# Optimization experiments

Hardware: AMD Instinct MI355X
Metric: run time of the kernel (lower is better)

Reference implementation:

```python
import jax, jax.numpy as jnp
import numpy as np
import math

H = 16          # n_head
N_EMBD = 1024
EPS = 1e-5      # torch LayerNorm default


def setup_inputs() -> dict:
    key = jax.random.key(0)
    ks = jax.random.split(key, 6)
    B, T, C = 2, 2048, 1024
    x = jax.random.normal(ks[0], (B, T, C), dtype=jnp.float32)
    s = 0.02  # GPT-2 style init scale keeps softmax logits sane
    Wq = jax.random.normal(ks[1], (C, N_EMBD), dtype=jnp.float32) * s
    Wk = jax.random.normal(ks[2], (C, N_EMBD), dtype=jnp.float32) * s
    Wv = jax.random.normal(ks[3], (C, N_EMBD), dtype=jnp.float32) * s
    Wo = jax.random.normal(ks[4], (N_EMBD, C), dtype=jnp.float32) * s
    return {
        "x": x,
        "Wq": Wq, "bq": jnp.zeros((N_EMBD,), jnp.float32),
        "Wk": Wk, "bk": jnp.zeros((N_EMBD,), jnp.float32),
        "Wv": Wv, "bv": jnp.zeros((N_EMBD,), jnp.float32),
        "Wo": Wo, "bo": jnp.zeros((C,), jnp.float32),
        "gamma": jnp.ones((C,), jnp.float32),
        "beta": jnp.zeros((C,), jnp.float32),
    }


def reference(x, Wq, bq, Wk, bk, Wv, bv, Wo, bo, gamma, beta):
    B, T, _ = x.shape
    Dh = N_EMBD // H
    # projections -> (B, H, T, Dh)
    def split_heads(y):
        return y.reshape(B, T, H, Dh).transpose(0, 2, 1, 3)
    q = split_heads(x @ Wq + bq)
    k = split_heads(x @ Wk + bk)
    v = split_heads(x @ Wv + bv)
    # naive causal attention: explicit (B,H,T,T) scores
    att = jnp.einsum("bhtd,bhsd->bhts", q, k) * (1.0 / math.sqrt(Dh))
    causal = jnp.tril(jnp.ones((T, T), dtype=bool))
    att = jnp.where(causal[None, None], att, -jnp.inf)
    att = jax.nn.softmax(att, axis=-1)
    o = jnp.einsum("bhts,bhsd->bhtd", att, v)
    o = o.transpose(0, 2, 1, 3).reshape(B, T, N_EMBD)
    y = o @ Wo + bo
    # LayerNorm (dropout is identity at p=0 / eval)
    mu = jnp.mean(y, axis=-1, keepdims=True)
    var = jnp.var(y, axis=-1, keepdims=True)
    return (y - mu) * jax.lax.rsqrt(var + EPS) * gamma + beta
```

## Files before the change

kernel.cpp:

```cpp
#include <hip/hip_runtime.h>
#include <stdint.h>
#include <stddef.h>

typedef __attribute__((ext_vector_type(8))) short short8;
typedef __attribute__((ext_vector_type(4))) float f32x4;
typedef __attribute__((ext_vector_type(16))) float f32x16;
typedef __attribute__((ext_vector_type(4))) unsigned short us4;
typedef __attribute__((ext_vector_type(4))) unsigned u32x4;

#define DEVI static __device__ __forceinline__

DEVI unsigned short f2bf(float f) {
  unsigned u = __builtin_bit_cast(unsigned, f);
  u += 0x7FFFu + ((u >> 16) & 1u);
  return (unsigned short)(u >> 16);
}

DEVI float bf2f(unsigned short u) {
  return __builtin_bit_cast(float, ((unsigned)u) << 16);
}

DEVI f32x4 mfma16(short8 a, short8 b, f32x4 c) {
  return __builtin_amdgcn_mfma_f32_16x16x32_bf16(a, b, c, 0, 0, 0);
}

DEVI f32x16 mfma32(short8 a, short8 b, f32x16 c) {
  return __builtin_amdgcn_mfma_f32_32x32x16_bf16(a, b, c, 0, 0, 0);
}

DEVI unsigned cvtpk(float lo, float hi) {
  unsigned r;
  asm("v_cvt_pk_bf16_f32 %0, %1, %2" : "=v"(r) : "v"(lo), "v"(hi));
  return r;
}

DEVI void plswap(unsigned& a, unsigned& b) {
  asm("v_permlane32_swap_b32 %0, %1" : "+v"(a), "+v"(b));
}

DEVI float ex2(float x) {
  float r;
  asm("v_exp_f32 %0, %1" : "=v"(r) : "v"(x));
  return r;
}

DEVI f32x16 zero16() {
  f32x16 z;
#pragma unroll
  for (int i = 0; i < 16; ++i) z[i] = 0.f;
  return z;
}

DEVI void glds16(const void* g, void* l) {
  __builtin_amdgcn_global_load_lds(
      (const __attribute__((address_space(1))) void*)g,
      (__attribute__((address_space(3))) void*)l, 16, 0, 0);
}

__global__ __launch_bounds__(256) void k_cvt_x(const float* __restrict__ x,
                                               unsigned short* __restrict__ xb) {
  size_t i = ((size_t)blockIdx.x * 256 + threadIdx.x) * 8;
  f32x4 a = *(const f32x4*)(x + i);
  f32x4 b = *(const f32x4*)(x + i + 4);
  short8 v;
#pragma unroll
  for (int j = 0; j < 4; ++j) {
    v[j] = (short)f2bf(a[j]);
    v[4 + j] = (short)f2bf(b[j]);
  }
  *(short8*)(xb + i) = v;
}

__global__ __launch_bounds__(256) void k_twT4(const float* __restrict__ W0,
                                              const float* __restrict__ W1,
                                              const float* __restrict__ W2,
                                              const float* __restrict__ W3,
                                              unsigned short* __restrict__ WT) {
  __shared__ float tile[64][65];
  const int z = blockIdx.z;
  const float* W = (z == 0) ? W0 : (z == 1) ? W1 : (z == 2) ? W2 : W3;
  unsigned short* out = WT + (size_t)z * 1024 * 1024;
  const int n0 = blockIdx.x * 64, k0 = blockIdx.y * 64;
  const int t = threadIdx.x, rr = t >> 4, cc = (t & 15) * 4;
#pragma unroll
  for (int i = 0; i < 4; ++i) {
    int row = i * 16 + rr;
    f32x4 v = *(const f32x4*)(W + (size_t)(k0 + row) * 1024 + n0 + cc);
#pragma unroll
    for (int j = 0; j < 4; ++j) tile[row][cc + j] = v[j];
  }
  __syncthreads();
#pragma unroll
  for (int i = 0; i < 4; ++i) {
    int nrow = i * 16 + rr;
    us4 u;
#pragma unroll
    for (int j = 0; j < 4; ++j) u[j] = f2bf(tile[cc + j][nrow]);
    *(us4*)(out + (size_t)(n0 + nrow) * 1024 + k0 + cc) = u;
  }
}

template <bool SWAP>
DEVI void gemm_core2(const unsigned short* __restrict__ A,
                     const unsigned short* __restrict__ Bt,
                     int mt, int nt, char* lds, f32x4 (&acc)[4][4]) {
  const int t = threadIdx.x;
  const int l = t & 63, c = l & 15, g = l >> 4;
  const int w = t >> 6, wr = w >> 1, wc = w & 1;
  const int srow = t >> 3;
  const int sxor = (((t & 7) ^ (srow & 7))) * 8;
  const unsigned short* Ab = A + (size_t)(mt * 128 + srow) * 1024 + sxor;
  const unsigned short* Bb = Bt + (size_t)(nt * 128 + srow) * 1024 + sxor;
  const int key = (c & 7);

  auto STAGE = [&](int kt, int buf) {
    char* lb = lds + buf * 32768;
#pragma unroll
    for (int i = 0; i < 4; ++i) {
      glds16(Ab + (size_t)i * 32 * 1024 + kt * 64, lb + i * 4096 + t * 16);
      glds16(Bb + (size_t)i * 32 * 1024 + kt * 64, lb + 16384 + i * 4096 + t * 16);
    }
  };

  STAGE(0, 0);
  asm volatile("s_waitcnt vmcnt(0)" ::: "memory");
  __builtin_amdgcn_s_barrier();
  asm volatile("" ::: "memory");
  for (int kt = 0; kt < 16; ++kt) {
    const int cur = kt & 1;
    if (kt < 15) STAGE(kt + 1, cur ^ 1);
    const char* lb = lds + cur * 32768;
#pragma unroll
    for (int ks = 0; ks < 2; ++ks) {
      short8 af[4], bfr[4];
#pragma unroll
      for (int m = 0; m < 4; ++m)
        af[m] = *(const short8*)(lb + (wr * 64 + m * 16 + c) * 128 +
                                 ((ks * 4 + g) ^ key) * 16);
#pragma unroll
      for (int n = 0; n < 4; ++n)
        bfr[n] = *(const short8*)(lb + 16384 + (wc * 64 + n * 16 + c) * 128 +
                                  ((ks * 4 + g) ^ key) * 16);
#pragma unroll
      for (int m = 0; m < 4; ++m)
#pragma unroll
        for (int n = 0; n < 4; ++n)
          acc[m][n] = SWAP ? mfma16(bfr[n], af[m], acc[m][n])
                           : mfma16(af[m], bfr[n], acc[m][n]);
    }
    asm volatile("s_waitcnt vmcnt(0)" ::: "memory");
    __builtin_amdgcn_s_barrier();
    asm volatile("" ::: "memory");
  }
}

DEVI void gemm_core5(const unsigned short* __restrict__ A,
                     const unsigned short* __restrict__ Bt,
                     int mt, int pt, char* lds, f32x4 (&acc)[8][3]) {
  const int t = threadIdx.x;
  const int l = t & 63, c = l & 15, g = l >> 4;
  const int w = t >> 6, wm = w >> 2, wn = w & 3;
  const int srow = t >> 3;
  const int sxor = ((t & 7) ^ (srow & 7)) * 8;
  const unsigned short* Ab = A + (size_t)(mt * 256 + srow) * 1024 + sxor;
  const unsigned short* Bb = Bt + (size_t)(pt * 192 + srow) * 1024 + sxor;
  const int key = c & 7;

  auto STAGE = [&](int kt, int buf) {
    char* lb = lds + buf * 57344;
#pragma unroll
    for (int i = 0; i < 4; ++i)
      glds16(Ab + (size_t)(i * 64) * 1024 + kt * 64, lb + i * 8192 + t * 16);
#pragma unroll
    for (int i = 0; i < 3; ++i)
      glds16(Bb + (size_t)(i * 64) * 1024 + kt * 64, lb + 32768 + i * 8192 + t * 16);
  };

  STAGE(0, 0);
  asm volatile("s_waitcnt vmcnt(0)" ::: "memory");
  __builtin_amdgcn_s_barrier();
  asm volatile("" ::: "memory");
  for (int kt = 0; kt < 16; ++kt) {
    const int cur = kt & 1;
    if (kt < 15) STAGE(kt + 1, cur ^ 1);
    const char* la = lds + cur * 57344;
    const char* lbB = la + 32768;
    short8 bf[3][2];
#pragma unroll
    for (int fc = 0; fc < 3; ++fc)
#pragma unroll
      for (int ks = 0; ks < 2; ++ks) {
        int brow = wn * 48 + fc * 16 + c;
        bf[fc][ks] = *(const short8*)(lbB + brow * 128 + (((ks * 4 + g) ^ key) * 16));
      }
#pragma unroll
    for (int p = 0; p < 4; ++p) {
      short8 af[2][2];
#pragma unroll
      for (int r2 = 0; r2 < 2; ++r2)
#pragma unroll
        for (int ks = 0; ks < 2; ++ks) {
          int arow = wm * 128 + (2 * p + r2) * 16 + c;
          af[r2][ks] = *(const short8*)(la + arow * 128 + (((ks * 4 + g) ^ key) * 16));
        }
      __builtin_amdgcn_s_setprio(1);
#pragma unroll
      for (int ks = 0; ks < 2; ++ks)
#pragma unroll
        for (int r2 = 0; r2 < 2; ++r2)
#pragma unroll
          for (int fc = 0; fc < 3; ++fc)
            acc[2 * p + r2][fc] = mfma16(bf[fc][ks], af[r2][ks], acc[2 * p + r2][fc]);
      __builtin_amdgcn_s_setprio(0);
    }
    asm volatile("s_waitcnt vmcnt(0)" ::: "memory");
    __builtin_amdgcn_s_barrier();
    asm volatile("" ::: "memory");
  }
}

__global__ __launch_bounds__(512) void k_gemm_qkv3(
    const unsigned short* __restrict__ A,
    const unsigned short* __restrict__ Wf,
    const float* __restrict__ b0, const float* __restrict__ b1, const float* __restrict__ b2,
    unsigned short* __restrict__ O0, unsigned short* __restrict__ O1,
    unsigned short* __restrict__ O2) {
  extern __shared__ char lds[];
  const int mt = blockIdx.x, pt = blockIdx.y;
  f32x4 acc[8][3];
#pragma unroll
  for (int m = 0; m < 8; ++m)
#pragma unroll
    for (int n = 0; n < 3; ++n) acc[m][n] = (f32x4){0.f, 0.f, 0.f, 0.f};
  gemm_core5(A, Wf, mt, pt, lds, acc);
  const int t = threadIdx.x, l = t & 63, c = l & 15, g = l >> 4;
  const int w = t >> 6, wm = w >> 2, wn = w & 3;
#pragma unroll
  for (int fc = 0; fc < 3; ++fc) {
    int colg3 = pt * 192 + wn * 48 + fc * 16 + 4 * g;
    int z = colg3 >> 10, colc = colg3 & 1023;
    const float* bias = (z == 0) ? b0 : (z == 1) ? b1 : b2;
    f32x4 bv4 = *(const f32x4*)(bias + colc);
    int h = colc >> 6, d = colc & 63;
    if (z < 2) {
      unsigned short* out = (z == 0) ? O0 : O1;
      const float sc = (z == 0) ? 0.18033688011f : 1.0f;
#pragma unroll
      for (int fr = 0; fr < 8; ++fr) {
        int rowg = mt * 256 + wm * 128 + fr * 16 + c;
        int b = rowg >> 11, tt = rowg & 2047;
        us4 u;
#pragma unroll
        for (int r = 0; r < 4; ++r) u[r] = f2bf((acc[fr][fc][r] + bv4[r]) * sc);
        *(us4*)(out + ((size_t)(b * 16 + h) * 2048 + tt) * 64 + d) = u;
      }
    } else {
#pragma unroll
      for (int fr = 0; fr < 8; ++fr) {
        int rowg = mt * 256 + wm * 128 + fr * 16 + c;
        int b = rowg >> 11, tt = rowg & 2047;
        size_t base = ((size_t)(b * 16 + h) * 64 + d) * 2048 + tt;
#pragma unroll
        for (int r = 0; r < 4; ++r)
          O2[base + (size_t)r * 2048] = f2bf(acc[fr][fc][r] + bv4[r]);
      }
    }
  }
}

__global__ __launch_bounds__(256) void k_gemm_proj(const unsigned short* __restrict__ A,
                                                   const unsigned short* __restrict__ Bt,
                                                   const float* __restrict__ bias,
                                                   unsigned short* __restrict__ Yb) {
  __shared__ char lds[65536];
  f32x4 acc[4][4];
#pragma unroll
  for (int m = 0; m < 4; ++m)
#pragma unroll
    for (int n = 0; n < 4; ++n) acc[m][n] = (f32x4){0.f, 0.f, 0.f, 0.f};
  const int lin = blockIdx.y * 32 + blockIdx.x;
  const int nt = lin & 7, mt = lin >> 3;
  gemm_core2<true>(A, Bt, mt, nt, lds, acc);
  const int t = threadIdx.x, l = t & 63, c = l & 15, g = l >> 4;
  const int w = t >> 6, wr = w >> 1, wc = w & 1;
#pragma unroll
  for (int n = 0; n < 4; ++n) {
    int colb = nt * 128 + wc * 64 + n * 16 + 4 * g;
    f32x4 bv4 = *(const f32x4*)(bias + colb);
#pragma unroll
    for (int m = 0; m < 4; ++m) {
      int rowg = mt * 128 + wr * 64 + m * 16 + c;
      us4 u;
#pragma unroll
      for (int r = 0; r < 4; ++r) u[r] = f2bf(acc[m][n][r] + bv4[r]);
      *(us4*)(Yb + (size_t)rowg * 1024 + colb) = u;
    }
  }
}

__global__ __launch_bounds__(256) void k_attn9(const unsigned short* __restrict__ Q,
                                               const unsigned short* __restrict__ K,
                                               const unsigned short* __restrict__ VT,
                                               unsigned short* __restrict__ O,
                                               unsigned short* __restrict__ P,
                                               float* __restrict__ ML) {
  __shared__ char lds[32768];
  const int bid = blockIdx.x;
  int qt, c0, NT, mode, bh;
  if (bid < 256) {
    mode = 1; qt = 8 + (bid >> 5); c0 = 0; NT = 16; bh = bid & 31;
  } else {
    int rem = bid - 256;
    int lvl = rem >> 6;
    int sub = rem & 63;
    bh = sub & 31;
    if (sub < 32) { mode = 0; qt = 7 - lvl;  c0 = 0;  NT = 2 * qt + 2; }
    else          { mode = 2; qt = 15 - lvl; c0 = 16; NT = 2 * qt - 14; }
  }
  const int t = threadIdx.x;
  const int w = t >> 6, l = t & 63;
  const int lq = l & 31, hi = l >> 5;
  const int q0 = qt * 128 + w * 32;
  const size_t kbase = (size_t)bh * 2048 * 64;
  const size_t vbase = (size_t)bh * 64 * 2048;
  const int srow = t >> 3;
  const int sx = ((t & 7) ^ (srow & 7)) * 8;
  const int my_nt = (mode == 1) ? 16 : (2 * qt + 1 + (w >> 1) - c0);

  short8 qf[4];
#pragma unroll
  for (int ds = 0; ds < 4; ++ds)
    qf[ds] = *(const short8*)(Q + kbase + (size_t)(q0 + lq) * 64 + 16 * ds + 8 * hi);

  auto STAGE = [&](int ktg, int buf) {
    const unsigned short* Kt = K + kbase + (size_t)ktg * 4096;
    const unsigned short* Vt = VT + vbase + ktg * 64;
    char* lb = lds + buf * 16384;
#pragma unroll
    for (int i = 0; i < 2; ++i) {
      int row = i * 32 + srow;
      glds16(Kt + (size_t)row * 64 + sx, lb + i * 4096 + t * 16);
      glds16(Vt + (size_t)row * 2048 + sx, lb + 8192 + i * 4096 + t * 16);
    }
  };

  f32x16 oacc[2];
  oacc[0] = zero16();
  oacc[1] = zero16();
  float l_s = 0.f;
  const int rx = lq & 7;

  STAGE(c0, 0);
  for (int kt = 0; kt < NT; ++kt) {
    asm volatile("s_waitcnt vmcnt(0)" ::: "memory");
    __builtin_amdgcn_s_barrier();
    asm volatile("" ::: "memory");
    if (kt + 1 < NT) STAGE(c0 + kt + 1, (kt + 1) & 1);
    if (kt < my_nt) {
      const char* lb = lds + (kt & 1) * 16384;
      const int kv0 = (c0 + kt) * 64;
      short8 kf0[4], kf1[4];
#pragma unroll
      for (int ds = 0; ds < 4; ++ds) {
        int blk = ((ds * 2 + hi) ^ rx) * 16;
        kf0[ds] = *(const short8*)(lb + lq * 128 + blk);
        kf1[ds] = *(const short8*)(lb + (lq + 32) * 128 + blk);
      }
      f32x16 st0 = zero16(), st1 = zero16();
      __builtin_amdgcn_s_setprio(1);
#pragma unroll
      for (int ds = 0; ds < 4; ++ds) {
        st0 = mfma32(kf0[ds], qf[ds], st0);
        st1 = mfma32(kf1[ds], qf[ds], st1);
      }
      __builtin_amdgcn_s_setprio(0);
      short8 vf[2][4];
#pragma unroll
      for (int fd = 0; fd < 2; ++fd) {
        int d = fd * 32 + lq;
#pragma unroll
        for (int s = 0; s < 4; ++s)
          vf[fd][s] = *(const short8*)(lb + 8192 + d * 128 + (((s * 2 + hi) ^ rx) * 16));
      }
      if (mode != 1 && kt == my_nt - 1) {
        const int qg = q0 + lq;
#pragma unroll
        for (int r = 0; r < 16; ++r) {
          int kr = kv0 + (r & 3) + 8 * (r >> 2) + 4 * hi;
          if (kr > qg) st0[r] = -1e30f;
          if (kr + 32 > qg) st1[r] = -1e30f;
        }
      }
      unsigned Wp[2][4][2];
      float gs[8];
#pragma unroll
      for (int f = 0; f < 2; ++f)
#pragma unroll
        for (int m4 = 0; m4 < 4; ++m4) {
          float p0 = ex2((f ? st1 : st0)[4 * m4 + 0]);
          float p1 = ex2((f ? st1 : st0)[4 * m4 + 1]);
          float p2 = ex2((f ? st1 : st0)[4 * m4 + 2]);
          float p3 = ex2((f ? st1 : st0)[4 * m4 + 3]);
          gs[f * 4 + m4] = (p0 + p1) + (p2 + p3);
          Wp[f][m4][0] = cvtpk(p0, p1);
          Wp[f][m4][1] = cvtpk(p2, p3);
        }
      l_s += ((gs[0] + gs[1]) + (gs[2] + gs[3])) + ((gs[4] + gs[5]) + (gs[6] + gs[7]));
      __builtin_amdgcn_s_setprio(1);
#pragma unroll
      for (int s = 0; s < 4; ++s) {
        const int f = s >> 1, s2 = s & 1;
        unsigned a0 = Wp[f][2 * s2][0], b0 = Wp[f][2 * s2 + 1][0];
        unsigned a1 = Wp[f][2 * s2][1], b1 = Wp[f][2 * s2 + 1][1];
        plswap(a0, b0);
        plswap(a1, b1);
        u32x4 pw = {a0, a1, b0, b1};
        short8 pf = __builtin_bit_cast(short8, pw);
        oacc[0] = mfma32(vf[0][s], pf, oacc[0]);
        oacc[1] = mfma32(vf[1][s], pf, oacc[1]);
      }
      __builtin_amdgcn_s_setprio(0);
    }
  }
  l_s += __shfl_xor(l_s, 32, 64);
  if (mode == 0) {
    const float inv = 1.0f / l_s;
    const int b = bh >> 4, h = bh & 15;
    unsigned short* orow = O + ((size_t)b * 2048 + q0 + lq) * 1024 + h * 64 + 4 * hi;
#pragma unroll
    for (int f = 0; f < 2; ++f)
#pragma unroll
      for (int m4 = 0; m4 < 4; ++m4) {
        us4 u;
#pragma unroll
        for (int rr = 0; rr < 4; ++rr) u[rr] = f2bf(oacc[f][4 * m4 + rr] * inv);
        *(us4*)(orow + f * 32 + m4 * 8) = u;
      }
  } else {
    const int pid = ((qt - 8) * 32 + bh) * 2 + (mode - 1);
    const int row = w * 32 + lq;
    unsigned short* prow = P + (size_t)pid * 8192 + row * 64 + 4 * hi;
#pragma unroll
    for (int f = 0; f < 2; ++f)
#pragma unroll
      for (int m4 = 0; m4 < 4; ++m4) {
        us4 u;
#pragma unroll
        for (int rr = 0; rr < 4; ++rr) u[rr] = f2bf(oacc[f][4 * m4 + rr]);
        *(us4*)(prow + f * 32 + m4 * 8) = u;
      }
    if (hi == 0) {
      ML[pid * 256 + row] = 0.f;
      ML[pid * 256 + 128 + row] = l_s;
    }
  }
}

__global__ __launch_bounds__(128) void k_merge(const unsigned short* __restrict__ P,
                                               const float* __restrict__ ML,
                                               unsigned short* __restrict__ O) {
  const int blk = blockIdx.x;
  const int qt = 8 + (blk >> 5), bh = blk & 31;
  const int pidA = ((qt - 8) * 32 + bh) * 2, pidB = pidA + 1;
  const int r = threadIdx.x;
  float mA = ML[pidA * 256 + r], lA = ML[pidA * 256 + 128 + r];
  float mB = ML[pidB * 256 + r], lB = ML[pidB * 256 + 128 + r];
  float mM = fmaxf(mA, mB);
  float wA = ex2(mA - mM), wB = ex2(mB - mM);
  float inv = 1.f / (lA * wA + lB * wB);
  wA *= inv;
  wB *= inv;
  const unsigned short* pa = P + (size_t)pidA * 8192 + r * 64;
  const unsigned short* pb = P + (size_t)pidB * 8192 + r * 64;
  const int b = bh >> 4, h = bh & 15, q = qt * 128 + r;
  unsigned short* orow = O + ((size_t)b * 2048 + q) * 1024 + h * 64;
#pragma unroll
  for (int j = 0; j < 8; ++j) {
    short8 a = *(const short8*)(pa + j * 8);
    short8 c = *(const short8*)(pb + j * 8);
    short8 o;
#pragma unroll
    for (int k = 0; k < 8; ++k)
      o[k] = (short)f2bf(bf2f((unsigned short)a[k]) * wA +
                         bf2f((unsigned short)c[k]) * wB);
    *(short8*)(orow + j * 8) = o;
  }
}

__global__ __launch_bounds__(256) void k_ln(const unsigned short* __restrict__ Yb,
                                            const float* __restrict__ gamma,
                                            const float* __restrict__ beta,
                                            float* __restrict__ out) {
  __shared__ float red[8];
  const int row = blockIdx.x, t = threadIdx.x, w = t >> 6, l = t & 63;
  us4 vb = *(const us4*)(Yb + (size_t)row * 1024 + t * 4);
  f32x4 v;
#pragma unroll
  for (int j = 0; j < 4; ++j) v[j] = bf2f(vb[j]);
  float s = v[0] + v[1] + v[2] + v[3];
  float ss = v[0] * v[0] + v[1] * v[1] + v[2] * v[2] + v[3] * v[3];
#pragma unroll
  for (int d = 1; d < 64; d <<= 1) {
    s += __shfl_xor(s, d, 64);
    ss += __shfl_xor(ss, d, 64);
  }
  if (l == 0) {
    red[w] = s;
    red[4 + w] = ss;
  }
  __syncthreads();
  s = red[0] + red[1] + red[2] + red[3];
  ss = red[4] + red[5] + red[6] + red[7];
  float mean = s * (1.f / 1024.f);
  float var = ss * (1.f / 1024.f) - mean * mean;
  float rstd = rsqrtf(var + 1e-5f);
  f32x4 gv = *(const f32x4*)(gamma + t * 4);
  f32x4 bv = *(const f32x4*)(beta + t * 4);
  f32x4 ov;
#pragma unroll
  for (int j = 0; j < 4; ++j) ov[j] = (v[j] - mean) * rstd * gv[j] + bv[j];
  *(f32x4*)(out + (size_t)row * 1024 + t * 4) = ov;
}

extern "C" void kernel_launch(void* const* d_in, const int* in_sizes, int n_in,
                              void* d_out, int out_size, void* d_ws, size_t ws_size,
                              hipStream_t stream) {
  (void)in_sizes; (void)n_in; (void)out_size; (void)ws_size;
  const float* x = (const float*)d_in[0];
  const float* Wq = (const float*)d_in[1];
  const float* bq = (const float*)d_in[2];
  const float* Wk = (const float*)d_in[3];
  const float* bk = (const float*)d_in[4];
  const float* Wv = (const float*)d_in[5];
  const float* bv = (const float*)d_in[6];
  const float* Wo = (const float*)d_in[7];
  const float* bo = (const float*)d_in[8];
  const float* gamma = (const float*)d_in[9];
  const float* beta = (const float*)d_in[10];
  char* ws = (char*)d_ws;
  const size_t MB = 1024 * 1024;
  unsigned short* xb = (unsigned short*)(ws);
  unsigned short* WT = (unsigned short*)(ws + 8 * MB);
  unsigned short* WoT = (unsigned short*)(ws + 14 * MB);
  unsigned short* Qb = (unsigned short*)(ws + 16 * MB);
  unsigned short* Kb = (unsigned short*)(ws + 24 * MB);
  unsigned short* VTb = (unsigned short*)(ws + 32 * MB);
  unsigned short* Ob = (unsigned short*)(ws + 40 * MB);
  unsigned short* Yb = (unsigned short*)(ws + 16 * MB);
  unsigned short* Pp = (unsigned short*)(ws);
  float* MLp = (float*)(ws + 8 * MB);

  k_cvt_x<<<2048, 256, 0, stream>>>(x, xb);
  k_twT4<<<dim3(16, 16, 4), 256, 0, stream>>>(Wq, Wk, Wv, Wo, WT);
  k_gemm_qkv3<<<dim3(16, 16), 512, 114688, stream>>>(xb, WT, bq, bk, bv, Qb, Kb, VTb);
  k_attn9<<<768, 256, 0, stream>>>(Qb, Kb, VTb, Ob, Pp, MLp);
  k_merge<<<256, 128, 0, stream>>>(Pp, MLp, Ob);
  k_gemm_proj<<<dim3(32, 8), 256, 0, stream>>>(Ob, WoT, bo, Yb);
  k_ln<<<4096, 256, 0, stream>>>(Yb, gamma, beta, (float*)d_out);
}
```

Baseline: 105.9 us.

## Retile QKV and output-projection GEMMs with triple-buffered LDS prefetch

The QKV GEMM is retiled from 256x192 tiles to 256x128 tiles, so each block handles a single projection (Q, K or V). This lets the V-transpose epilogue use a swapped MFMA operand order and write vectorized 4-wide stores instead of scalar strided ones. Both GEMMs move from double buffering to a three-stage LDS pipeline that prefetches two k-tiles ahead, with a partial vmcnt wait so loads overlap compute. The output projection now uses 512-thread blocks with 4x2 fragments per wave, which raises LDS use to 144KB and 96KB per block and may reduce how many blocks fit per CU.

```diff
diff --git a/kernel.cpp b/kernel.cpp
--- a/kernel.cpp
+++ b/kernel.cpp
@@ -101,198 +101,217 @@
 }
 
 template <bool SWAP>
-DEVI void gemm_core2(const unsigned short* __restrict__ A,
+DEVI void gemm_core6(const unsigned short* __restrict__ A,
                      const unsigned short* __restrict__ Bt,
-                     int mt, int nt, char* lds, f32x4 (&acc)[4][4]) {
+                     int mt, int ntz, char* lds, f32x4 (&acc)[4][4]) {
   const int t = threadIdx.x;
   const int l = t & 63, c = l & 15, g = l >> 4;
-  const int w = t >> 6, wr = w >> 1, wc = w & 1;
+  const int w = t >> 6, wm = w >> 1, wn = w & 1;
   const int srow = t >> 3;
-  const int sxor = (((t & 7) ^ (srow & 7))) * 8;
-  const unsigned short* Ab = A + (size_t)(mt * 128 + srow) * 1024 + sxor;
-  const unsigned short* Bb = Bt + (size_t)(nt * 128 + srow) * 1024 + sxor;
-  const int key = (c & 7);
+  const int sxor = ((t & 7) ^ (srow & 7)) * 8;
+  const unsigned short* Ab = A + (size_t)(mt * 256 + srow) * 1024 + sxor;
+  const unsigned short* Bb = Bt + (size_t)(ntz * 128 + srow) * 1024 + sxor;
+  const int key = c & 7;
 
   auto STAGE = [&](int kt, int buf) {
-    char* lb = lds + buf * 32768;
-#pragma unroll
-    for (int i = 0; i < 4; ++i) {
-      glds16(Ab + (size_t)i * 32 * 1024 + kt * 64, lb + i * 4096 + t * 16);
-      glds16(Bb + (size_t)i * 32 * 1024 + kt * 64, lb + 16384 + i * 4096 + t * 16);
-    }
+    char* lb = lds + buf * 49152;
+#pragma unroll
+    for (int i = 0; i < 4; ++i)
+      glds16(Ab + (size_t)(i * 64) * 1024 + kt * 64, lb + i * 8192 + t * 16);
+#pragma unroll
+    for (int i = 0; i < 2; ++i)
+      glds16(Bb + (size_t)(i * 64) * 1024 + kt * 64, lb + 32768 + i * 8192 + t * 16);
   };
 
   STAGE(0, 0);
-  asm volatile("s_waitcnt vmcnt(0)" ::: "memory");
+  STAGE(1, 1);
+  asm volatile("s_waitcnt vmcnt(6)" ::: "memory");
   __builtin_amdgcn_s_barrier();
   asm volatile("" ::: "memory");
   for (int kt = 0; kt < 16; ++kt) {
-    const int cur = kt & 1;
-    if (kt < 15) STAGE(kt + 1, cur ^ 1);
-    const char* lb = lds + cur * 32768;
-#pragma unroll
-    for (int ks = 0; ks < 2; ++ks) {
-      short8 af[4], bfr[4];
-#pragma unroll
-      for (int m = 0; m < 4; ++m)
-        af[m] = *(const short8*)(lb + (wr * 64 + m * 16 + c) * 128 +
-                                 ((ks * 4 + g) ^ key) * 16);
-#pragma unroll
-      for (int n = 0; n < 4; ++n)
-        bfr[n] = *(const short8*)(lb + 16384 + (wc * 64 + n * 16 + c) * 128 +
-                                  ((ks * 4 + g) ^ key) * 16);
-#pragma unroll
-      for (int m = 0; m < 4; ++m)
-#pragma unroll
-        for (int n = 0; n < 4; ++n)
-          acc[m][n] = SWAP ? mfma16(bfr[n], af[m], acc[m][n])
-                           : mfma16(af[m], bfr[n], acc[m][n]);
-    }
-    asm volatile("s_waitcnt vmcnt(0)" ::: "memory");
+    if (kt + 2 < 16) STAGE(kt + 2, (kt + 2) % 3);
+    const char* la = lds + (kt % 3) * 49152;
+    const char* lbB = la + 32768;
+    short8 bf[4][2];
+#pragma unroll
+    for (int fc = 0; fc < 4; ++fc)
+#pragma unroll
+      for (int ks = 0; ks < 2; ++ks)
+        bf[fc][ks] = *(const short8*)(lbB + (wn * 64 + fc * 16 + c) * 128 +
+                                      (((ks * 4 + g) ^ key) * 16));
+#pragma unroll
+    for (int p = 0; p < 2; ++p) {
+      short8 af[2][2];
+#pragma unroll
+      for (int r2 = 0; r2 < 2; ++r2)
+#pragma unroll
+        for (int ks = 0; ks < 2; ++ks)
+          af[r2][ks] = *(const short8*)(la + (wm * 64 + (2 * p + r2) * 16 + c) * 128 +
+                                        (((ks * 4 + g) ^ key) * 16));
+      __builtin_amdgcn_s_setprio(1);
+#pragma unroll
+      for (int ks = 0; ks < 2; ++ks)
+#pragma unroll
+        for (int r2 = 0; r2 < 2; ++r2)
+#pragma unroll
+          for (int fc = 0; fc < 4; ++fc)
+            acc[2 * p + r2][fc] = SWAP
+                ? mfma16(bf[fc][ks], af[r2][ks], acc[2 * p + r2][fc])
+                : mfma16(af[r2][ks], bf[fc][ks], acc[2 * p + r2][fc]);
+      __builtin_amdgcn_s_setprio(0);
+    }
+    if (kt + 2 < 16) {
+      asm volatile("s_waitcnt vmcnt(6)" ::: "memory");
+    } else {
+      asm volatile("s_waitcnt vmcnt(0)" ::: "memory");
+    }
     __builtin_amdgcn_s_barrier();
     asm volatile("" ::: "memory");
   }
 }
 
-DEVI void gemm_core5(const unsigned short* __restrict__ A,
-                     const unsigned short* __restrict__ Bt,
-                     int mt, int pt, char* lds, f32x4 (&acc)[8][3]) {
-  const int t = threadIdx.x;
-  const int l = t & 63, c = l & 15, g = l >> 4;
-  const int w = t >> 6, wm = w >> 2, wn = w & 3;
-  const int srow = t >> 3;
-  const int sxor = ((t & 7) ^ (srow & 7)) * 8;
-  const unsigned short* Ab = A + (size_t)(mt * 256 + srow) * 1024 + sxor;
-  const unsigned short* Bb = Bt + (size_t)(pt * 192 + srow) * 1024 + sxor;
-  const int key = c & 7;
-
-  auto STAGE = [&](int kt, int buf) {
-    char* lb = lds + buf * 57344;
-#pragma unroll
-    for (int i = 0; i < 4; ++i)
-      glds16(Ab + (size_t)(i * 64) * 1024 + kt * 64, lb + i * 8192 + t * 16);
-#pragma unroll
-    for (int i = 0; i < 3; ++i)
-      glds16(Bb + (size_t)(i * 64) * 1024 + kt * 64, lb + 32768 + i * 8192 + t * 16);
-  };
-
-  STAGE(0, 0);
-  asm volatile("s_waitcnt vmcnt(0)" ::: "memory");
-  __builtin_amdgcn_s_barrier();
-  asm volatile("" ::: "memory");
-  for (int kt = 0; kt < 16; ++kt) {
-    const int cur = kt & 1;
-    if (kt < 15) STAGE(kt + 1, cur ^ 1);
-    const char* la = lds + cur * 57344;
-    const char* lbB = la + 32768;
-    short8 bf[3][2];
-#pragma unroll
-    for (int fc = 0; fc < 3; ++fc)
-#pragma unroll
-      for (int ks = 0; ks < 2; ++ks) {
-        int brow = wn * 48 + fc * 16 + c;
-        bf[fc][ks] = *(const short8*)(lbB + brow * 128 + (((ks * 4 + g) ^ key) * 16));
-      }
-#pragma unroll
-    for (int p = 0; p < 4; ++p) {
-      short8 af[2][2];
-#pragma unroll
-      for (int r2 = 0; r2 < 2; ++r2)
-#pragma unroll
-        for (int ks = 0; ks < 2; ++ks) {
-          int arow = wm * 128 + (2 * p + r2) * 16 + c;
-          af[r2][ks] = *(const short8*)(la + arow * 128 + (((ks * 4 + g) ^ key) * 16));
-        }
-      __builtin_amdgcn_s_setprio(1);
-#pragma unroll
-      for (int ks = 0; ks < 2; ++ks)
-#pragma unroll
-        for (int r2 = 0; r2 < 2; ++r2)
-#pragma unroll
-          for (int fc = 0; fc < 3; ++fc)
-            acc[2 * p + r2][fc] = mfma16(bf[fc][ks], af[r2][ks], acc[2 * p + r2][fc]);
-      __builtin_amdgcn_s_setprio(0);
-    }
-    asm volatile("s_waitcnt vmcnt(0)" ::: "memory");
-    __builtin_amdgcn_s_barrier();
-    asm volatile("" ::: "memory");
-  }
-}
-
-__global__ __launch_bounds__(512) void k_gemm_qkv3(
+__global__ __launch_bounds__(512) void k_gemm_qkv4(
     const unsigned short* __restrict__ A,
     const unsigned short* __restrict__ Wf,
     const float* __restrict__ b0, const float* __restrict__ b1, const float* __restrict__ b2,
     unsigned short* __restrict__ O0, unsigned short* __restrict__ O1,
     unsigned short* __restrict__ O2) {
   extern __shared__ char lds[];
-  const int mt = blockIdx.x, pt = blockIdx.y;
-  f32x4 acc[8][3];
-#pragma unroll
-  for (int m = 0; m < 8; ++m)
-#pragma unroll
-    for (int n = 0; n < 3; ++n) acc[m][n] = (f32x4){0.f, 0.f, 0.f, 0.f};
-  gemm_core5(A, Wf, mt, pt, lds, acc);
+  const int ntz = blockIdx.x, mt = blockIdx.y;
+  const int z = ntz >> 3, ntl = ntz & 7;
+  const float* bias = (z == 0) ? b0 : (z == 1) ? b1 : b2;
+  f32x4 acc[4][4];
+#pragma unroll
+  for (int m = 0; m < 4; ++m)
+#pragma unroll
+    for (int n = 0; n < 4; ++n) acc[m][n] = (f32x4){0.f, 0.f, 0.f, 0.f};
+  const int t = threadIdx.x, l = t & 63, c = l & 15, g = l >> 4;
+  const int w = t >> 6, wm = w >> 1, wn = w & 1;
+  if (z < 2) {
+    gemm_core6<true>(A, Wf, mt, ntz, lds, acc);
+    const float sc = (z == 0) ? 0.18033688011f : 1.0f;
+#pragma unroll
+    for (int fc = 0; fc < 4; ++fc) {
+      int colc = ntl * 128 + wn * 64 + fc * 16 + 4 * g;
+      f32x4 bv4 = *(const f32x4*)(bias + colc);
+      int h = colc >> 6, d = colc & 63;
+      unsigned short* out = (z == 0) ? O0 : O1;
+#pragma unroll
+      for (int fr = 0; fr < 4; ++fr) {
+        int rowg = mt * 256 + wm * 64 + fr * 16 + c;
+        int b = rowg >> 11, tt = rowg & 2047;
+        us4 u;
+#pragma unroll
+        for (int r = 0; r < 4; ++r) u[r] = f2bf((acc[fr][fc][r] + bv4[r]) * sc);
+        *(us4*)(out + ((size_t)(b * 16 + h) * 2048 + tt) * 64 + d) = u;
+      }
+    }
+  } else {
+    gemm_core6<false>(A, Wf, mt, ntz, lds, acc);
+#pragma unroll
+    for (int fc = 0; fc < 4; ++fc) {
+      int colg = ntl * 128 + wn * 64 + fc * 16 + c;
+      float bvv = bias[colg];
+      int h = colg >> 6, d = colg & 63;
+#pragma unroll
+      for (int fr = 0; fr < 4; ++fr) {
+        int rowg = mt * 256 + wm * 64 + fr * 16 + 4 * g;
+        int b = rowg >> 11, tt = rowg & 2047;
+        us4 u;
+#pragma unroll
+        for (int r = 0; r < 4; ++r) u[r] = f2bf(acc[fr][fc][r] + bvv);
+        *(us4*)(O2 + ((size_t)(b * 16 + h) * 64 + d) * 2048 + tt) = u;
+      }
+    }
+  }
+}
+
+DEVI void gemm_core7(const unsigned short* __restrict__ A,
+                     const unsigned short* __restrict__ Bt,
+                     int mt, int nt, char* lds, f32x4 (&acc)[4][2]) {
+  const int t = threadIdx.x;
+  const int l = t & 63, c = l & 15, g = l >> 4;
+  const int w = t >> 6, wm = w >> 2, wn = w & 3;
+  const int srow = t >> 3;
+  const int sxor = ((t & 7) ^ (srow & 7)) * 8;
+  const unsigned short* Ab = A + (size_t)(mt * 128 + srow) * 1024 + sxor;
+  const unsigned short* Bb = Bt + (size_t)(nt * 128 + srow) * 1024 + sxor;
+  const int key = c & 7;
+
+  auto STAGE = [&](int kt, int buf) {
+    char* lb = lds + buf * 32768;
+#pragma unroll
+    for (int i = 0; i < 2; ++i) {
+      glds16(Ab + (size_t)(i * 64) * 1024 + kt * 64, lb + i * 8192 + t * 16);
+      glds16(Bb + (size_t)(i * 64) * 1024 + kt * 64, lb + 16384 + i * 8192 + t * 16);
+    }
+  };
+
+  STAGE(0, 0);
+  STAGE(1, 1);
+  asm volatile("s_waitcnt vmcnt(4)" ::: "memory");
+  __builtin_amdgcn_s_barrier();
+  asm volatile("" ::: "memory");
+  for (int kt = 0; kt < 16; ++kt) {
+    if (kt + 2 < 16) STAGE(kt + 2, (kt + 2) % 3);
+    const char* la = lds + (kt % 3) * 32768;
+    const char* lbB = la + 16384;
+    short8 bf[2][2], af[4][2];
+#pragma unroll
+    for (int fc = 0; fc < 2; ++fc)
+#pragma unroll
+      for (int ks = 0; ks < 2; ++ks)
+        bf[fc][ks] = *(const short8*)(lbB + (wn * 32 + fc * 16 + c) * 128 +
+                                      (((ks * 4 + g) ^ key) * 16));
+#pragma unroll
+    for (int fr = 0; fr < 4; ++fr)
+#pragma unroll
+      for (int ks = 0; ks < 2; ++ks)
+        af[fr][ks] = *(const short8*)(la + (wm * 64 + fr * 16 + c) * 128 +
+                                      (((ks * 4 + g) ^ key) * 16));
+    __builtin_amdgcn_s_setprio(1);
+#pragma unroll
+    for (int ks = 0; ks < 2; ++ks)
+#pragma unroll
+      for (int fr = 0; fr < 4; ++fr)
+#pragma unroll
+        for (int fc = 0; fc < 2; ++fc)
+          acc[fr][fc] = mfma16(bf[fc][ks], af[fr][ks], acc[fr][fc]);
+    __builtin_amdgcn_s_setprio(0);
+    if (kt + 2 < 16) {
+      asm volatile("s_waitcnt vmcnt(4)" ::: "memory");
+    } else {
+      asm volatile("s_waitcnt vmcnt(0)" ::: "memory");
+    }
+    __builtin_amdgcn_s_barrier();
+    asm volatile("" ::: "memory");
+  }
+}
+
+__global__ __launch_bounds__(512) void k_gemm_proj2(const unsigned short* __restrict__ A,
+                                                    const unsigned short* __restrict__ Bt,
+                                                    const float* __restrict__ bias,
+                                                    unsigned short* __restrict__ Yb) {
+  extern __shared__ char lds[];
+  f32x4 acc[4][2];
+#pragma unroll
+  for (int m = 0; m < 4; ++m)
+#pragma unroll
+    for (int n = 0; n < 2; ++n) acc[m][n] = (f32x4){0.f, 0.f, 0.f, 0.f};
+  const int nt = blockIdx.x, mt = blockIdx.y;
+  gemm_core7(A, Bt, mt, nt, lds, acc);
   const int t = threadIdx.x, l = t & 63, c = l & 15, g = l >> 4;
   const int w = t >> 6, wm = w >> 2, wn = w & 3;
 #pragma unroll
-  for (int fc = 0; fc < 3; ++fc) {
-    int colg3 = pt * 192 + wn * 48 + fc * 16 + 4 * g;
-    int z = colg3 >> 10, colc = colg3 & 1023;
-    const float* bias = (z == 0) ? b0 : (z == 1) ? b1 : b2;
-    f32x4 bv4 = *(const f32x4*)(bias + colc);
-    int h = colc >> 6, d = colc & 63;
-    if (z < 2) {
-      unsigned short* out = (z == 0) ? O0 : O1;
-      const float sc = (z == 0) ? 0.18033688011f : 1.0f;
-#pragma unroll
-      for (int fr = 0; fr < 8; ++fr) {
-        int rowg = mt * 256 + wm * 128 + fr * 16 + c;
-        int b = rowg >> 11, tt = rowg & 2047;
-        us4 u;
-#pragma unroll
-        for (int r = 0; r < 4; ++r) u[r] = f2bf((acc[fr][fc][r] + bv4[r]) * sc);
-        *(us4*)(out + ((size_t)(b * 16 + h) * 2048 + tt) * 64 + d) = u;
-      }
-    } else {
-#pragma unroll
-      for (int fr = 0; fr < 8; ++fr) {
-        int rowg = mt * 256 + wm * 128 + fr * 16 + c;
-        int b = rowg >> 11, tt = rowg & 2047;
-        size_t base = ((size_t)(b * 16 + h) * 64 + d) * 2048 + tt;
-#pragma unroll
-        for (int r = 0; r < 4; ++r)
-          O2[base + (size_t)r * 2048] = f2bf(acc[fr][fc][r] + bv4[r]);
-      }
-    }
-  }
-}
-
-__global__ __launch_bounds__(256) void k_gemm_proj(const unsigned short* __restrict__ A,
-                                                   const unsigned short* __restrict__ Bt,
-                                                   const float* __restrict__ bias,
-                                                   unsigned short* __restrict__ Yb) {
-  __shared__ char lds[65536];
-  f32x4 acc[4][4];
-#pragma unroll
-  for (int m = 0; m < 4; ++m)
-#pragma unroll
-    for (int n = 0; n < 4; ++n) acc[m][n] = (f32x4){0.f, 0.f, 0.f, 0.f};
-  const int lin = blockIdx.y * 32 + blockIdx.x;
-  const int nt = lin & 7, mt = lin >> 3;
-  gemm_core2<true>(A, Bt, mt, nt, lds, acc);
-  const int t = threadIdx.x, l = t & 63, c = l & 15, g = l >> 4;
-  const int w = t >> 6, wr = w >> 1, wc = w & 1;
-#pragma unroll
-  for (int n = 0; n < 4; ++n) {
-    int colb = nt * 128 + wc * 64 + n * 16 + 4 * g;
+  for (int fc = 0; fc < 2; ++fc) {
+    int colb = nt * 128 + wn * 32 + fc * 16 + 4 * g;
     f32x4 bv4 = *(const f32x4*)(bias + colb);
 #pragma unroll
-    for (int m = 0; m < 4; ++m) {
-      int rowg = mt * 128 + wr * 64 + m * 16 + c;
+    for (int fr = 0; fr < 4; ++fr) {
+      int rowg = mt * 128 + wm * 64 + fr * 16 + c;
       us4 u;
 #pragma unroll
-      for (int r = 0; r < 4; ++r) u[r] = f2bf(acc[m][n][r] + bv4[r]);
+      for (int r = 0; r < 4; ++r) u[r] = f2bf(acc[fr][fc][r] + bv4[r]);
       *(us4*)(Yb + (size_t)rowg * 1024 + colb) = u;
     }
   }
@@ -552,9 +571,9 @@
 
   k_cvt_x<<<2048, 256, 0, stream>>>(x, xb);
   k_twT4<<<dim3(16, 16, 4), 256, 0, stream>>>(Wq, Wk, Wv, Wo, WT);
-  k_gemm_qkv3<<<dim3(16, 16), 512, 114688, stream>>>(xb, WT, bq, bk, bv, Qb, Kb, VTb);
+  k_gemm_qkv4<<<dim3(24, 16), 512, 147456, stream>>>(xb, WT, bq, bk, bv, Qb, Kb, VTb);
   k_attn9<<<768, 256, 0, stream>>>(Qb, Kb, VTb, Ob, Pp, MLp);
   k_merge<<<256, 128, 0, stream>>>(Pp, MLp, Ob);
-  k_gemm_proj<<<dim3(32, 8), 256, 0, stream>>>(Ob, WoT, bo, Yb);
+  k_gemm_proj2<<<dim3(8, 32), 512, 98304, stream>>>(Ob, WoT, bo, Yb);
   k_ln<<<4096, 256, 0, stream>>>(Yb, gamma, beta, (float*)d_out);
 }
```

New measurement: 119.8 us. 1.13x slower.

## Split attention KV work into three chunks and rebalance block scheduling

Applied to the files above, without the earlier changes.

The upper query tiles (qt 8-15) now have their unmasked KV range split into two 8-tile chunks plus a masked diagonal chunk, so each tile produces three partials instead of two. The grid grows from 768 to 1024 blocks, ordered so the long diagonal blocks launch first and the short ones fill in at the end. Because every partial uses the same fixed (zero) max, the merge kernel just sums three partials and divides by the summed denominators, with no exponential reweighting. The aim is shorter per-block work and a smaller tail on the CUs, paid for with more partial-output traffic and an extra read per element in the merge.

```diff
diff --git a/kernel.cpp b/kernel.cpp
--- a/kernel.cpp
+++ b/kernel.cpp
@@ -298,24 +298,29 @@
   }
 }
 
-__global__ __launch_bounds__(256) void k_attn9(const unsigned short* __restrict__ Q,
-                                               const unsigned short* __restrict__ K,
-                                               const unsigned short* __restrict__ VT,
-                                               unsigned short* __restrict__ O,
-                                               unsigned short* __restrict__ P,
-                                               float* __restrict__ ML) {
+__global__ __launch_bounds__(256) void k_attn11(const unsigned short* __restrict__ Q,
+                                                const unsigned short* __restrict__ K,
+                                                const unsigned short* __restrict__ VT,
+                                                unsigned short* __restrict__ O,
+                                                unsigned short* __restrict__ P,
+                                                float* __restrict__ L) {
   __shared__ char lds[32768];
   const int bid = blockIdx.x;
-  int qt, c0, NT, mode, bh;
+  int qt, c0, NT, mode, bh, ci = 0;
   if (bid < 256) {
-    mode = 1; qt = 8 + (bid >> 5); c0 = 0; NT = 16; bh = bid & 31;
+    int g = bid >> 5, q2 = g >> 1;
+    bh = bid & 31;
+    if ((g & 1) == 0) { mode = 0; qt = 7 - q2;  c0 = 0;  NT = 2 * qt + 2; }
+    else              { mode = 1; qt = 15 - q2; c0 = 16; NT = 2 * qt - 14; ci = 2; }
+  } else if (bid < 768) {
+    int i = bid - 256, idx = i >> 5;
+    bh = i & 31;
+    mode = 1; qt = 8 + (idx >> 1); ci = idx & 1; c0 = ci * 8; NT = 8;
   } else {
-    int rem = bid - 256;
-    int lvl = rem >> 6;
-    int sub = rem & 63;
-    bh = sub & 31;
-    if (sub < 32) { mode = 0; qt = 7 - lvl;  c0 = 0;  NT = 2 * qt + 2; }
-    else          { mode = 2; qt = 15 - lvl; c0 = 16; NT = 2 * qt - 14; }
+    int i = bid - 768, g = i >> 5, q2 = g >> 1;
+    bh = i & 31;
+    if ((g & 1) == 0) { mode = 0; qt = 3 - q2;  c0 = 0;  NT = 2 * qt + 2; }
+    else              { mode = 1; qt = 11 - q2; c0 = 16; NT = 2 * qt - 14; ci = 2; }
   }
   const int t = threadIdx.x;
   const int w = t >> 6, l = t & 63;
@@ -325,7 +330,8 @@
   const size_t vbase = (size_t)bh * 64 * 2048;
   const int srow = t >> 3;
   const int sx = ((t & 7) ^ (srow & 7)) * 8;
-  const int my_nt = (mode == 1) ? 16 : (2 * qt + 1 + (w >> 1) - c0);
+  const bool nomask = (mode == 1 && ci < 2);
+  const int my_nt = nomask ? NT : (2 * qt + 1 + (w >> 1) - c0);
 
   short8 qf[4];
 #pragma unroll
@@ -382,7 +388,7 @@
         for (int s = 0; s < 4; ++s)
           vf[fd][s] = *(const short8*)(lb + 8192 + d * 128 + (((s * 2 + hi) ^ rx) * 16));
       }
-      if (mode != 1 && kt == my_nt - 1) {
+      if (!nomask && kt == my_nt - 1) {
         const int qg = q0 + lq;
 #pragma unroll
         for (int r = 0; r < 16; ++r) {
@@ -437,7 +443,7 @@
         *(us4*)(orow + f * 32 + m4 * 8) = u;
       }
   } else {
-    const int pid = ((qt - 8) * 32 + bh) * 2 + (mode - 1);
+    const int pid = ((qt - 8) * 32 + bh) * 3 + ci;
     const int row = w * 32 + lq;
     unsigned short* prow = P + (size_t)pid * 8192 + row * 64 + 4 * hi;
 #pragma unroll
@@ -449,40 +455,32 @@
         for (int rr = 0; rr < 4; ++rr) u[rr] = f2bf(oacc[f][4 * m4 + rr]);
         *(us4*)(prow + f * 32 + m4 * 8) = u;
       }
-    if (hi == 0) {
-      ML[pid * 256 + row] = 0.f;
-      ML[pid * 256 + 128 + row] = l_s;
-    }
-  }
-}
-
-__global__ __launch_bounds__(128) void k_merge(const unsigned short* __restrict__ P,
-                                               const float* __restrict__ ML,
-                                               unsigned short* __restrict__ O) {
+    if (hi == 0) L[pid * 128 + row] = l_s;
+  }
+}
+
+__global__ __launch_bounds__(128) void k_merge3(const unsigned short* __restrict__ P,
+                                                const float* __restrict__ L,
+                                                unsigned short* __restrict__ O) {
   const int blk = blockIdx.x;
   const int qt = 8 + (blk >> 5), bh = blk & 31;
-  const int pidA = ((qt - 8) * 32 + bh) * 2, pidB = pidA + 1;
+  const int pid0 = ((qt - 8) * 32 + bh) * 3;
   const int r = threadIdx.x;
-  float mA = ML[pidA * 256 + r], lA = ML[pidA * 256 + 128 + r];
-  float mB = ML[pidB * 256 + r], lB = ML[pidB * 256 + 128 + r];
-  float mM = fmaxf(mA, mB);
-  float wA = ex2(mA - mM), wB = ex2(mB - mM);
-  float inv = 1.f / (lA * wA + lB * wB);
-  wA *= inv;
-  wB *= inv;
-  const unsigned short* pa = P + (size_t)pidA * 8192 + r * 64;
-  const unsigned short* pb = P + (size_t)pidB * 8192 + r * 64;
+  float inv = 1.f / (L[pid0 * 128 + r] + L[(pid0 + 1) * 128 + r] +
+                     L[(pid0 + 2) * 128 + r]);
+  const unsigned short* pa = P + (size_t)pid0 * 8192 + r * 64;
   const int b = bh >> 4, h = bh & 15, q = qt * 128 + r;
   unsigned short* orow = O + ((size_t)b * 2048 + q) * 1024 + h * 64;
 #pragma unroll
   for (int j = 0; j < 8; ++j) {
     short8 a = *(const short8*)(pa + j * 8);
-    short8 c = *(const short8*)(pb + j * 8);
+    short8 c = *(const short8*)(pa + 8192 + j * 8);
+    short8 e = *(const short8*)(pa + 16384 + j * 8);
     short8 o;
 #pragma unroll
     for (int k = 0; k < 8; ++k)
-      o[k] = (short)f2bf(bf2f((unsigned short)a[k]) * wA +
-                         bf2f((unsigned short)c[k]) * wB);
+      o[k] = (short)f2bf((bf2f((unsigned short)a[k]) + bf2f((unsigned short)c[k]) +
+                          bf2f((unsigned short)e[k])) * inv);
     *(short8*)(orow + j * 8) = o;
   }
 }
@@ -548,13 +546,13 @@
   unsigned short* Ob = (unsigned short*)(ws + 40 * MB);
   unsigned short* Yb = (unsigned short*)(ws + 16 * MB);
   unsigned short* Pp = (unsigned short*)(ws);
-  float* MLp = (float*)(ws + 8 * MB);
+  float* Lp = (float*)(ws + 12 * MB);
 
   k_cvt_x<<<2048, 256, 0, stream>>>(x, xb);
   k_twT4<<<dim3(16, 16, 4), 256, 0, stream>>>(Wq, Wk, Wv, Wo, WT);
   k_gemm_qkv3<<<dim3(16, 16), 512, 114688, stream>>>(xb, WT, bq, bk, bv, Qb, Kb, VTb);
-  k_attn9<<<768, 256, 0, stream>>>(Qb, Kb, VTb, Ob, Pp, MLp);
-  k_merge<<<256, 128, 0, stream>>>(Pp, MLp, Ob);
+  k_attn11<<<1024, 256, 0, stream>>>(Qb, Kb, VTb, Ob, Pp, Lp);
+  k_merge3<<<256, 128, 0, stream>>>(Pp, Lp, Ob);
   k_gemm_proj<<<dim3(32, 8), 256, 0, stream>>>(Ob, WoT, bo, Yb);
   k_ln<<<4096, 256, 0, stream>>>(Yb, gamma, beta, (float*)d_out);
 }
```

Result: no change. 104.7 us (-1.1%).
